# Optimization experiments

Hardware: AMD Instinct MI355X
Metric: run time of the kernel (lower is better)

## Reference

```python
import jax, jax.numpy as jnp
import numpy as np

H = 32
DECAY = 0.9


def setup_inputs() -> dict:
    key = jax.random.key(0)
    ks = jax.random.split(key, 6)
    B, T, D = 8, 4096, 1024
    x = jax.random.normal(ks[0], (B, T, D), dtype=jnp.float32)
    s = 1.0 / np.sqrt(D)
    Wv = jax.random.normal(ks[1], (D, D), dtype=jnp.float32) * s
    bv = jax.random.normal(ks[2], (D,), dtype=jnp.float32) * s
    Wo = jax.random.normal(ks[3], (D, D), dtype=jnp.float32) * s
    bo = jax.random.normal(ks[4], (D,), dtype=jnp.float32) * s
    w = jnp.asarray(DECAY ** np.arange(H), dtype=jnp.float32)
    decay_w = w / jnp.sum(w)
    return {"x": x, "Wv": Wv, "bv": bv, "Wo": Wo, "bo": bo, "decay_w": decay_w}


def reference(x, Wv, bv, Wo, bo, decay_w):
    # x: [B, T, D]. Original pads H zeros at front and unfolds windows of size H
    # with stride 1, producing T+1 windows: window t covers x[t-H .. t-1].
    # value_proj is linear and applied to every window copy, so it commutes with
    # the fixed-weight sum: attended = (sum_i w_i * x_window_i) @ Wv^T + bv*sum(w).
    B, T, D = x.shape
    Hlen = decay_w.shape[0]
    x_pad = jnp.pad(x, ((0, 0), (Hlen, 0), (0, 0)))  # [B, T+H, D]
    # Depthwise 1D conv over time with the (shared) decay kernel.
    kernel = jnp.broadcast_to(decay_w[:, None, None], (Hlen, 1, D))  # [W, I=1, O=D]
    s = jax.lax.conv_general_dilated(
        x_pad, kernel, window_strides=(1,), padding="VALID",
        dimension_numbers=("NWC", "WIO", "NWC"), feature_group_count=D,
    )  # [B, T+1, D]
    attended = s @ Wv.T + bv * jnp.sum(decay_w)
    return attended @ Wo.T + bo  # [B, T+1, D]
```

## Files before the change

### kernel.cpp

```cpp
#include <hip/hip_runtime.h>
#include <stdint.h>

#define D_DIM 1024
#define T_DIM 4096
#define B_DIM 8
#define M_REAL (B_DIM * (T_DIM + 1))
#define M_MAIN 32768

typedef short short8 __attribute__((ext_vector_type(8)));
typedef float floatx4 __attribute__((ext_vector_type(4)));

typedef const __attribute__((address_space(1))) void* gptr_t;
typedef __attribute__((address_space(3))) void* lptr_t;

__device__ __forceinline__ ushort f2bf(float f) {
  union { float f; uint32_t u; } v; v.f = f;
  uint32_t r = v.u + 0x7FFF + ((v.u >> 16) & 1);
  return (ushort)(r >> 16);
}
__device__ __forceinline__ float bf2f(ushort b) {
  union { uint32_t u; float f; } v; v.u = ((uint32_t)b) << 16; return v.f;
}

__global__ __launch_bounds__(256) void gemm128_kernel(
    const ushort* __restrict__ A, const ushort* __restrict__ Bm,
    float* __restrict__ C, const float* __restrict__ bias)
{
  __shared__ ushort As[128][64];
  __shared__ ushort Bs[128][64];
  const int tid  = threadIdx.x;
  const int wave = tid >> 6;
  const int lane = tid & 63;
  const int wm = wave >> 1, wn = wave & 1;
  const int l15 = lane & 15, lhi = lane >> 4;
  const int rsw = (l15 & 7) << 4;

  const int bid = blockIdx.x;
  const int wg  = (bid & 7) * 256 + (bid >> 3);
  const int n0 = (wg & 7) * 128;
  const int m0 = (wg >> 3) * 128;

  const int srow = tid >> 3;
  const int ksw  = ((tid & 7) ^ (srow & 7)) * 8;
  const ushort* Ab = A  + (size_t)(m0 + srow) * D_DIM + ksw;
  const ushort* Bb = Bm + (size_t)(n0 + srow) * D_DIM + ksw;

  floatx4 acc[4][4] = {};

  for (int k0 = 0; k0 < D_DIM; k0 += 64) {
#pragma unroll
    for (int q = 0; q < 4; ++q)
      __builtin_amdgcn_global_load_lds((gptr_t)(Ab + k0 + (size_t)q * 32 * D_DIM),
          (lptr_t)((char*)&As[0][0] + (q * 256 + wave * 64) * 16), 16, 0, 0);
#pragma unroll
    for (int q = 0; q < 4; ++q)
      __builtin_amdgcn_global_load_lds((gptr_t)(Bb + k0 + (size_t)q * 32 * D_DIM),
          (lptr_t)((char*)&Bs[0][0] + (q * 256 + wave * 64) * 16), 16, 0, 0);
    __syncthreads();

#pragma unroll
    for (int kk = 0; kk < 2; ++kk) {
      short8 af[4], bfrg[4];
#pragma unroll
      for (int i = 0; i < 4; ++i) {
        const int oa = ((wm * 64 + i * 16 + l15) * 128 + kk * 64 + lhi * 16) ^ rsw;
        const int ob = ((wn * 64 + i * 16 + l15) * 128 + kk * 64 + lhi * 16) ^ rsw;
        af[i]   = *(const short8*)((const char*)&As[0][0] + oa);
        bfrg[i] = *(const short8*)((const char*)&Bs[0][0] + ob);
      }
#pragma unroll
      for (int mi = 0; mi < 4; ++mi)
#pragma unroll
        for (int ni = 0; ni < 4; ++ni)
          acc[mi][ni] = __builtin_amdgcn_mfma_f32_16x16x32_bf16(
              af[mi], bfrg[ni], acc[mi][ni], 0, 0, 0);
    }
    __syncthreads();
  }

#pragma unroll
  for (int mi = 0; mi < 4; ++mi)
#pragma unroll
    for (int ni = 0; ni < 4; ++ni) {
      const int gn = n0 + wn * 64 + ni * 16 + l15;
      const float bia = bias[gn];
#pragma unroll
      for (int j = 0; j < 4; ++j) {
        const int gm = m0 + wm * 64 + mi * 16 + lhi * 4 + j;
        C[(size_t)gm * D_DIM + gn] = acc[mi][ni][j] + bia;
      }
    }
}

__global__ __launch_bounds__(256) void tail_gemv_kernel(
    const ushort* __restrict__ S, const ushort* __restrict__ Wf,
    const float* __restrict__ cvec, float* __restrict__ out)
{
  const int wavei = threadIdx.x >> 6, lane = threadIdx.x & 63;
  const int c = blockIdx.x * 4 + wavei;
  float acc[8] = {};
  for (int i = 0; i < 16; ++i) {
    const int k = i * 64 + lane;
    const float wv = bf2f(Wf[(size_t)c * D_DIM + k]);
#pragma unroll
    for (int r = 0; r < 8; ++r)
      acc[r] += wv * bf2f(S[(size_t)(M_MAIN + r) * D_DIM + k]);
  }
#pragma unroll
  for (int r = 0; r < 8; ++r) {
#pragma unroll
    for (int off = 32; off; off >>= 1) acc[r] += __shfl_xor(acc[r], off, 64);
  }
  if (lane == 0) {
    const float bia = cvec[c];
#pragma unroll
    for (int r = 0; r < 8; ++r)
      out[(size_t)(M_MAIN + r) * D_DIM + c] = acc[r] + bia;
  }
}

__global__ __launch_bounds__(256) void gemm_bt_kernel(
    const ushort* __restrict__ A, const ushort* __restrict__ Bm,
    ushort* __restrict__ Cb, int K, int N)
{
  __shared__ ushort As[128][64];
  __shared__ ushort Bs[128][64];
  const int tid  = threadIdx.x;
  const int wave = tid >> 6;
  const int lane = tid & 63;
  const int wm = wave >> 1, wn = wave & 1;
  const int n0 = blockIdx.x * 128, m0 = blockIdx.y * 128;
  const int l15 = lane & 15, lhi = lane >> 4;

  floatx4 acc[4][4] = {};

  const int srow = tid >> 3;
  const int sk8  = (tid & 7) * 8;
  const ushort* Ab = A  + (size_t)(m0 + srow) * K + sk8;
  const ushort* Bb = Bm + (size_t)(n0 + srow) * K + sk8;

  for (int k0 = 0; k0 < K; k0 += 64) {
#pragma unroll
    for (int q = 0; q < 4; ++q)
      __builtin_amdgcn_global_load_lds((gptr_t)(Ab + k0 + (size_t)q * 32 * K),
          (lptr_t)((char*)&As[0][0] + (q * 256 + wave * 64) * 16), 16, 0, 0);
#pragma unroll
    for (int q = 0; q < 4; ++q)
      __builtin_amdgcn_global_load_lds((gptr_t)(Bb + k0 + (size_t)q * 32 * K),
          (lptr_t)((char*)&Bs[0][0] + (q * 256 + wave * 64) * 16), 16, 0, 0);
    __syncthreads();

#pragma unroll
    for (int kk = 0; kk < 2; ++kk) {
      short8 af[4], bfrg[4];
#pragma unroll
      for (int i = 0; i < 4; ++i) {
        af[i]   = *(const short8*)(&As[wm * 64 + i * 16 + l15][kk * 32 + lhi * 8]);
        bfrg[i] = *(const short8*)(&Bs[wn * 64 + i * 16 + l15][kk * 32 + lhi * 8]);
      }
#pragma unroll
      for (int mi = 0; mi < 4; ++mi)
#pragma unroll
        for (int ni = 0; ni < 4; ++ni)
          acc[mi][ni] = __builtin_amdgcn_mfma_f32_16x16x32_bf16(
              af[mi], bfrg[ni], acc[mi][ni], 0, 0, 0);
    }
    __syncthreads();
  }

#pragma unroll
  for (int mi = 0; mi < 4; ++mi)
#pragma unroll
    for (int ni = 0; ni < 4; ++ni) {
      const int gn = n0 + wn * 64 + ni * 16 + l15;
#pragma unroll
      for (int j = 0; j < 4; ++j) {
        const int gm = m0 + wm * 64 + mi * 16 + lhi * 4 + j;
        Cb[(size_t)gm * N + gn] = f2bf(acc[mi][ni][j]);
      }
    }
}

#define CTCH 128
__global__ __launch_bounds__(256) void conv_kernel(
    const float* __restrict__ x, const float* __restrict__ dw,
    ushort* __restrict__ S)
{
  const int b   = blockIdx.y;
  const int col = blockIdx.z * 256 + threadIdx.x;
  const int t0  = blockIdx.x * CTCH;

  float w[32];
#pragma unroll
  for (int i = 0; i < 32; ++i) w[i] = dw[i];
  const float rinv = w[0] / w[1];
  const float w31  = w[31];
  const float c0   = -w[0] * rinv;

  const float* xb = x + (size_t)b * T_DIM * D_DIM + col;
  ushort*      Sb = S + (size_t)b * (T_DIM + 1) * D_DIM + col;

  float prev[32], cur[32];
  float s;
  if (blockIdx.x == 0) {
#pragma unroll
    for (int i = 0; i < 32; ++i) prev[i] = 0.f;
    s = 0.f;
    Sb[0] = f2bf(0.f);
  } else {
#pragma unroll
    for (int i = 0; i < 32; ++i) prev[i] = xb[(size_t)(t0 - 32 + i) * D_DIM];
    s = 0.f;
#pragma unroll
    for (int i = 0; i < 32; ++i) s = __builtin_fmaf(w[i], prev[i], s);
  }

#pragma unroll 1
  for (int g = 0; g < 4; g += 2) {
#pragma unroll
    for (int i = 0; i < 32; ++i) cur[i] = xb[(size_t)(t0 + g * 32 + i) * D_DIM];
#pragma unroll
    for (int j = 0; j < 32; ++j) {
      s = __builtin_fmaf(s, rinv, __builtin_fmaf(prev[j], c0, w31 * cur[j]));
      Sb[(size_t)(t0 + g * 32 + 1 + j) * D_DIM] = f2bf(s);
    }
    s = 0.f;
#pragma unroll
    for (int i = 0; i < 32; ++i) s = __builtin_fmaf(w[i], cur[i], s);
#pragma unroll
    for (int i = 0; i < 32; ++i) prev[i] = xb[(size_t)(t0 + (g + 1) * 32 + i) * D_DIM];
#pragma unroll
    for (int j = 0; j < 32; ++j) {
      s = __builtin_fmaf(s, rinv, __builtin_fmaf(cur[j], c0, w31 * prev[j]));
      Sb[(size_t)(t0 + (g + 1) * 32 + 1 + j) * D_DIM] = f2bf(s);
    }
    s = 0.f;
#pragma unroll
    for (int i = 0; i < 32; ++i) s = __builtin_fmaf(w[i], prev[i], s);
  }
}

__global__ void convert_wo_kernel(const float* __restrict__ Wo, ushort* __restrict__ WoB) {
  const int i = blockIdx.x * 256 + threadIdx.x;
  const float4 v = ((const float4*)Wo)[i];
  ushort4 o = make_ushort4(f2bf(v.x), f2bf(v.y), f2bf(v.z), f2bf(v.w));
  *(ushort4*)(WoB + (size_t)i * 4) = o;
}

__global__ void transpose_wv_kernel(const float* __restrict__ Wv, ushort* __restrict__ WvT) {
  __shared__ float tile[32][33];
  const int tx = threadIdx.x;
  const int ty = threadIdx.y;
  const int c0 = blockIdx.x * 32;
  const int r0 = blockIdx.y * 32;
#pragma unroll
  for (int j = 0; j < 4; ++j)
    tile[ty + j * 8][tx] = Wv[(size_t)(r0 + ty + j * 8) * D_DIM + c0 + tx];
  __syncthreads();
#pragma unroll
  for (int j = 0; j < 4; ++j)
    WvT[(size_t)(c0 + ty + j * 8) * D_DIM + r0 + tx] = f2bf(tile[tx][ty + j * 8]);
}

__global__ void bias_kernel(const float* __restrict__ Wo, const float* __restrict__ bv,
                            const float* __restrict__ bo, const float* __restrict__ dw,
                            float* __restrict__ cvec) {
  const int j    = blockIdx.x * 4 + (threadIdx.x >> 6);
  const int lane = threadIdx.x & 63;
  float sumw = 0.f;
#pragma unroll
  for (int i = 0; i < 32; ++i) sumw += dw[i];
  float s = 0.f;
  for (int k = lane; k < D_DIM; k += 64) s += Wo[(size_t)j * D_DIM + k] * bv[k];
#pragma unroll
  for (int off = 32; off; off >>= 1) s += __shfl_xor(s, off, 64);
  if (lane == 0) cvec[j] = sumw * s + bo[j];
}

extern "C" void kernel_launch(void* const* d_in, const int* in_sizes, int n_in,
                              void* d_out, int out_size, void* d_ws, size_t ws_size,
                              hipStream_t stream) {
  const float* x  = (const float*)d_in[0];
  const float* Wv = (const float*)d_in[1];
  const float* bv = (const float*)d_in[2];
  const float* Wo = (const float*)d_in[3];
  const float* bo = (const float*)d_in[4];
  const float* dw = (const float*)d_in[5];
  float* out = (float*)d_out;

  char* ws = (char*)d_ws;
  ushort* S      = (ushort*)ws;
  ushort* WoB    = (ushort*)(ws + (size_t)M_REAL * D_DIM * 2);
  ushort* WvT    = WoB + (size_t)D_DIM * D_DIM;
  ushort* Wfused = WvT + (size_t)D_DIM * D_DIM;
  float*  cvec   = (float*)(Wfused + (size_t)D_DIM * D_DIM);

  convert_wo_kernel<<<dim3(D_DIM * D_DIM / 1024), dim3(256), 0, stream>>>(Wo, WoB);
  transpose_wv_kernel<<<dim3(32, 32), dim3(32, 8), 0, stream>>>(Wv, WvT);
  bias_kernel<<<dim3(256), dim3(256), 0, stream>>>(Wo, bv, bo, dw, cvec);

  gemm_bt_kernel<<<dim3(8, 8), dim3(256), 0, stream>>>(
      WoB, WvT, Wfused, D_DIM, D_DIM);

  conv_kernel<<<dim3(T_DIM / CTCH, B_DIM, 4), dim3(256), 0, stream>>>(x, dw, S);

  gemm128_kernel<<<dim3(2048), dim3(256), 0, stream>>>(S, Wfused, out, cvec);
  tail_gemv_kernel<<<dim3(256), dim3(256), 0, stream>>>(S, Wfused, cvec, out);
}
```

Measured before the change: 169.1 us.

## Replace main GEMM with 256x256-tile, 16-wave, triple-buffered pipelined kernel

The main bf16 GEMM moves from 128x128 tiles with 4 waves to 256x256 tiles with 16 waves per workgroup. The K-loop now uses a three-stage LDS ring of 32-wide K slices, fed by async global-to-LDS loads with explicit vmcnt waits, and raises wave priority around the MFMA blocks. The intent is to cut global traffic per flop and hide load latency behind compute. In exchange it uses 96KB of LDS and 1024-thread blocks, leaving only 512 workgroups, and it depends on hand-placed waits and barriers being correct.

```diff
diff --git a/kernel.cpp b/kernel.cpp
--- a/kernel.cpp
+++ b/kernel.cpp
@@ -6,6 +6,7 @@
 #define B_DIM 8
 #define M_REAL (B_DIM * (T_DIM + 1))
 #define M_MAIN 32768
+#define NWG 512
 
 typedef short short8 __attribute__((ext_vector_type(8)));
 typedef float floatx4 __attribute__((ext_vector_type(4)));
@@ -22,74 +23,108 @@
   union { uint32_t u; float f; } v; v.u = ((uint32_t)b) << 16; return v.f;
 }
 
-__global__ __launch_bounds__(256) void gemm128_kernel(
+#define BARRIER()  asm volatile("s_barrier" ::: "memory")
+#define WAIT_VM4() asm volatile("s_waitcnt vmcnt(4)" ::: "memory")
+#define WAIT_VM2() asm volatile("s_waitcnt vmcnt(2)" ::: "memory")
+#define WAIT_VM0() asm volatile("s_waitcnt vmcnt(0)" ::: "memory")
+#define WAIT_LGKM0() do { asm volatile("s_waitcnt lgkmcnt(0)" ::: "memory"); \
+                          __builtin_amdgcn_sched_barrier(0); } while (0)
+#define SP1() __builtin_amdgcn_s_setprio(1)
+#define SP0() __builtin_amdgcn_s_setprio(0)
+
+__global__ __launch_bounds__(1024) void gemm_w16_kernel(
     const ushort* __restrict__ A, const ushort* __restrict__ Bm,
     float* __restrict__ C, const float* __restrict__ bias)
 {
-  __shared__ ushort As[128][64];
-  __shared__ ushort Bs[128][64];
+  __shared__ char smem[98304];
   const int tid  = threadIdx.x;
   const int wave = tid >> 6;
   const int lane = tid & 63;
-  const int wm = wave >> 1, wn = wave & 1;
+  const int wm = wave >> 2, wn = wave & 3;
   const int l15 = lane & 15, lhi = lane >> 4;
-  const int rsw = (l15 & 7) << 4;
 
   const int bid = blockIdx.x;
-  const int wg  = (bid & 7) * 256 + (bid >> 3);
-  const int n0 = (wg & 7) * 128;
-  const int m0 = (wg >> 3) * 128;
-
-  const int srow = tid >> 3;
-  const int ksw  = ((tid & 7) ^ (srow & 7)) * 8;
-  const ushort* Ab = A  + (size_t)(m0 + srow) * D_DIM + ksw;
-  const ushort* Bb = Bm + (size_t)(n0 + srow) * D_DIM + ksw;
-
+  const int wg  = (bid & 7) * 64 + (bid >> 3);
+  const int n0 = (wg & 3) * 256;
+  const int m0 = (wg >> 2) * 256;
+
+  const int srow = tid >> 2;
+  const int ksw  = ((tid & 3) ^ ((tid >> 3) & 3)) * 8;
+  const ushort* Aq = A  + (size_t)(m0 + srow) * D_DIM + ksw;
+  const ushort* Bq = Bm + (size_t)(n0 + srow) * D_DIM + ksw;
+
+  const int xorc = (lhi ^ ((l15 >> 1) & 3)) * 16;
+  const int aoff = (wm * 64 + l15) * 64 + xorc;
+  const int boff = (wn * 64 + l15) * 64 + xorc;
+
+  short8 a[4], b[4];
   floatx4 acc[4][4] = {};
 
-  for (int k0 = 0; k0 < D_DIM; k0 += 64) {
-#pragma unroll
-    for (int q = 0; q < 4; ++q)
-      __builtin_amdgcn_global_load_lds((gptr_t)(Ab + k0 + (size_t)q * 32 * D_DIM),
-          (lptr_t)((char*)&As[0][0] + (q * 256 + wave * 64) * 16), 16, 0, 0);
-#pragma unroll
-    for (int q = 0; q < 4; ++q)
-      __builtin_amdgcn_global_load_lds((gptr_t)(Bb + k0 + (size_t)q * 32 * D_DIM),
-          (lptr_t)((char*)&Bs[0][0] + (q * 256 + wave * 64) * 16), 16, 0, 0);
-    __syncthreads();
-
-#pragma unroll
-    for (int kk = 0; kk < 2; ++kk) {
-      short8 af[4], bfrg[4];
-#pragma unroll
-      for (int i = 0; i < 4; ++i) {
-        const int oa = ((wm * 64 + i * 16 + l15) * 128 + kk * 64 + lhi * 16) ^ rsw;
-        const int ob = ((wn * 64 + i * 16 + l15) * 128 + kk * 64 + lhi * 16) ^ rsw;
-        af[i]   = *(const short8*)((const char*)&As[0][0] + oa);
-        bfrg[i] = *(const short8*)((const char*)&Bs[0][0] + ob);
+#define STAGE_W(PA, PB, S) do { \
+  __builtin_amdgcn_global_load_lds((gptr_t)(PA), \
+      (lptr_t)(smem + (S) * 16384 + wave * 1024), 16, 0, 0); \
+  __builtin_amdgcn_global_load_lds((gptr_t)(PB), \
+      (lptr_t)(smem + 49152 + (S) * 16384 + wave * 1024), 16, 0, 0); \
+} while (0)
+
+#define LDAB_W(S) do { \
+  _Pragma("unroll") \
+  for (int m = 0; m < 4; ++m) \
+    a[m] = *(const short8*)(smem + (S) * 16384 + aoff + m * 1024); \
+  _Pragma("unroll") \
+  for (int n = 0; n < 4; ++n) \
+    b[n] = *(const short8*)(smem + 49152 + (S) * 16384 + boff + n * 1024); \
+} while (0)
+
+#define MFMA_W() do { \
+  _Pragma("unroll") \
+  for (int m = 0; m < 4; ++m) \
+    _Pragma("unroll") \
+    for (int n = 0; n < 4; ++n) \
+      acc[m][n] = __builtin_amdgcn_mfma_f32_16x16x32_bf16( \
+          a[m], b[n], acc[m][n], 0, 0, 0); \
+} while (0)
+
+#define ITER_W(S0, S2, STG, VMW) do { \
+  if (STG) { STAGE_W(ApS, BpS, S2); ApS += 32; BpS += 32; } \
+  VMW; \
+  BARRIER(); \
+  LDAB_W(S0); \
+  WAIT_LGKM0(); \
+  SP1(); MFMA_W(); SP0(); \
+  BARRIER(); \
+} while (0)
+
+  STAGE_W(Aq, Bq, 0);
+  STAGE_W(Aq + 32, Bq + 32, 1);
+  const ushort* ApS = Aq + 64;
+  const ushort* BpS = Bq + 64;
+
+#pragma unroll 1
+  for (int it = 0; it < 10; ++it) {
+    ITER_W(0, 2, 1, WAIT_VM4());
+    ITER_W(1, 0, 1, WAIT_VM4());
+    ITER_W(2, 1, 1, WAIT_VM4());
+  }
+  ITER_W(0, 0, 0, WAIT_VM2());
+  ITER_W(1, 0, 0, WAIT_VM0());
+
+#pragma unroll
+  for (int m = 0; m < 4; ++m)
+#pragma unroll
+    for (int n = 0; n < 4; ++n) {
+      const int gn = n0 + wn * 64 + n * 16 + l15;
+      const float bia = bias[gn];
+#pragma unroll
+      for (int j = 0; j < 4; ++j) {
+        const int gm = m0 + wm * 64 + m * 16 + lhi * 4 + j;
+        C[(size_t)gm * D_DIM + gn] = acc[m][n][j] + bia;
       }
-#pragma unroll
-      for (int mi = 0; mi < 4; ++mi)
-#pragma unroll
-        for (int ni = 0; ni < 4; ++ni)
-          acc[mi][ni] = __builtin_amdgcn_mfma_f32_16x16x32_bf16(
-              af[mi], bfrg[ni], acc[mi][ni], 0, 0, 0);
-    }
-    __syncthreads();
-  }
-
-#pragma unroll
-  for (int mi = 0; mi < 4; ++mi)
-#pragma unroll
-    for (int ni = 0; ni < 4; ++ni) {
-      const int gn = n0 + wn * 64 + ni * 16 + l15;
-      const float bia = bias[gn];
-#pragma unroll
-      for (int j = 0; j < 4; ++j) {
-        const int gm = m0 + wm * 64 + mi * 16 + lhi * 4 + j;
-        C[(size_t)gm * D_DIM + gn] = acc[mi][ni][j] + bia;
-      }
-    }
+    }
+#undef STAGE_W
+#undef LDAB_W
+#undef MFMA_W
+#undef ITER_W
 }
 
 __global__ __launch_bounds__(256) void tail_gemv_kernel(
@@ -304,6 +339,6 @@
 
   conv_kernel<<<dim3(T_DIM / CTCH, B_DIM, 4), dim3(256), 0, stream>>>(x, dw, S);
 
-  gemm128_kernel<<<dim3(2048), dim3(256), 0, stream>>>(S, Wfused, out, cvec);
+  gemm_w16_kernel<<<dim3(NWG), dim3(1024), 0, stream>>>(S, Wfused, out, cvec);
   tail_gemv_kernel<<<dim3(256), dim3(256), 0, stream>>>(S, Wfused, cvec, out);
 }
```

New measurement: 167.2 us. Within noise of the previous version (-1.1%).
